# Kernel tuning notes

Hardware: AMD Instinct MI355X
Metric: run time of the kernel (lower is better)

## Reference

```python
import jax, jax.numpy as jnp
import numpy as np
from jax import lax

B, T, I, H = 64, 512, 256, 512


def _lstm_cell(inp, h, c, Wx, bx, Wh):
    # Wx: (4, in_dim, H), bx: (4, H), Wh: (4, H, H); gate order: i, f, o, g
    gates = jnp.einsum('bi,gio->bgo', inp, Wx) + jnp.einsum('bh,gho->bgo', h, Wh) + bx
    i_t = jax.nn.sigmoid(gates[:, 0])
    f_t = jax.nn.sigmoid(gates[:, 1])
    o_t = jax.nn.sigmoid(gates[:, 2])
    g_t = jnp.tanh(gates[:, 3])
    c_new = f_t * c + i_t * g_t
    h_new = o_t * jnp.tanh(c_new)
    return h_new, c_new


def setup_inputs() -> dict:
    key = jax.random.key(0)
    ks = jax.random.split(key, 9)
    s_i = 1.0 / np.sqrt(H)  # nn.Linear default init scale (uniform fan_in)
    s_x0 = 1.0 / np.sqrt(I)
    u = lambda k, shape, s: jax.random.uniform(k, shape, jnp.float32, -s, s)
    return {
        'x':   jax.random.normal(ks[0], (B, T, I), jnp.float32),
        'Wx0': u(ks[1], (4, I, H), s_x0),
        'bx0': u(ks[2], (4, H), s_x0),
        'Wh0': u(ks[3], (4, H, H), s_i),
        'Wx1': u(ks[4], (4, H, H), s_i),
        'bx1': u(ks[5], (4, H), s_i),
        'Wh1': u(ks[6], (4, H, H), s_i),
        'Wfc': u(ks[7], (H, 1), s_i),
        'bfc': u(ks[8], (1,), s_i),
    }


def reference(x, Wx0, bx0, Wh0, Wx1, bx1, Wh1, Wfc, bfc):
    b = x.shape[0]
    h = Wh0.shape[-1]
    zeros = jnp.zeros((b, h), x.dtype)
    carry0 = (zeros, zeros, zeros, zeros)  # h0, c0, h1, c1

    def step(carry, x_t):
        h0, c0, h1, c1 = carry
        h0, c0 = _lstm_cell(x_t, h0, c0, Wx0, bx0, Wh0)
        h1, c1 = _lstm_cell(h0, h1, c1, Wx1, bx1, Wh1)
        return (h0, c0, h1, c1), None

    x_t_major = jnp.swapaxes(x, 0, 1)  # (T, B, I)
    (h0, c0, h1, c1), _ = lax.scan(step, carry0, x_t_major)
    return h1 @ Wfc + bfc  # (B, 1)
```

## Files before the change

### kernel.cpp

```cpp
#include <hip/hip_runtime.h>
#include <stdint.h>

#define B_ 64
#define T_ 512
#define I_ 256
#define H_ 512
#define G0_ 128
#define G1_ 128
#define NTHR_ 512
#define D_ 8

typedef __attribute__((ext_vector_type(8))) short short8;
typedef __attribute__((ext_vector_type(4))) float float4v;
typedef __attribute__((ext_vector_type(4))) unsigned int uint4v;
typedef __attribute__((ext_vector_type(2))) unsigned int uint2v;

static_assert(sizeof(short8) == 16, "");

#define TILE_B 2048
#define SLOT_B ((size_t)4 * 16 * TILE_B)

__device__ __forceinline__ unsigned short f2bf(float x) {
  union { float f; uint32_t u; } v; v.f = x;
  uint32_t r = v.u + 0x7FFFu + ((v.u >> 16) & 1u);
  return (unsigned short)(r >> 16);
}
__device__ __forceinline__ float bf2f(unsigned short h) {
  union { uint32_t u; float f; } v; v.u = ((uint32_t)h) << 16; return v.f;
}
__device__ __forceinline__ void splitHL(float x, unsigned short& hi, unsigned short& lo) {
  hi = f2bf(x);
  lo = f2bf(x - bf2f(hi));
}

__device__ __forceinline__ size_t rbyte(int slot, int bg, int ht, int lane) {
  return ((size_t)slot * 64 + bg * 16 + ht) * TILE_B + (size_t)lane * 16;
}

__device__ __forceinline__ void wait_ge(const uint32_t* p, int tgt) {
  if (tgt <= 0) return;
  int it = 0;
  while ((int)__hip_atomic_load(p, __ATOMIC_RELAXED, __HIP_MEMORY_SCOPE_AGENT) < tgt) {
    __builtin_amdgcn_s_sleep(1);
    if (++it > 2000000) break;
  }
}

#define MFMA16(A, Bv, C) __builtin_amdgcn_mfma_f32_16x16x32_bf16(A, Bv, C, 0, 0, 0)

#define WAITV(n) do { \
    asm volatile("s_waitcnt vmcnt(" #n ")" ::: "memory"); \
    __builtin_amdgcn_sched_barrier(0); \
  } while (0)

template <int LAYER, bool FULL>
__device__ void run_layer(
    int a,
    const float* __restrict__ x,
    const float* __restrict__ Wxp, const float* __restrict__ bxp,
    const float* __restrict__ Whp,
    uint32_t* prog0, uint32_t* prog1,
    uint8_t* r0, uint8_t* r1,
    float* h1f,
    unsigned short* Wsh, float* red)
{
  constexpr int K1 = LAYER ? H_ : I_;
  constexpr int NT = (K1 + H_) / 32;
  constexpr int NTT = NT / 2;
  const int tid = threadIdx.x;
  const int lane = tid & 63;
  const int wid = tid >> 6;
  const int bg = wid & 3;
  const int kh = wid >> 2;
  const int qq = lane >> 4;
  const int cc = lane & 15;
  const int brow = bg * 16 + cc;

  short8 wlo[NTT];
  for (int pass = 0; pass < 2; ++pass) {
    for (int idx = tid; idx < NT * 512; idx += NTHR_) {
      int tile = idx >> 9, r = idx & 511, ln = r >> 3, j = r & 7;
      int k = tile * 32 + 4 * (ln >> 4) + (j & 3) + 16 * (j >> 2);
      int n = 4 * a + (ln & 3);
      int g = (ln & 15) >> 2;
      float wvv = (k < K1) ? Wxp[((size_t)g * K1 + k) * H_ + n]
                           : Whp[((size_t)g * H_ + (k - K1)) * H_ + n];
      unsigned short hi, lo; splitHL(wvv, hi, lo);
      Wsh[idx] = pass ? hi : lo;
    }
    __syncthreads();
    if (pass == 0) {
      #pragma unroll
      for (int tt = 0; tt < NTT; ++tt) {
        int tile = 2 * tt + kh;
        wlo[tt] = *(const short8*)(Wsh + tile * 512 + lane * 8);
      }
      __syncthreads();
    }
  }

  const float biasv = bxp[(size_t)(cc >> 2) * H_ + 4 * a + (cc & 3)];
  float cst[4] = {0.f, 0.f, 0.f, 0.f};

  uint32_t* myprog = LAYER ? prog1 : prog0;
  const bool ownw = FULL ? ((tid & 127) == a) : false;

  for (int t = 0; t < T_; ++t) {
    const int slotP = FULL ? t       : (t & (D_ - 1));
    const int slotC = FULL ? (t + 1) : ((t + 1) & (D_ - 1));
    float bv = (kh == 0) ? biasv : 0.f;
    float4v accA = {bv, bv, bv, bv};
    float4v accB = {0.f, 0.f, 0.f, 0.f};
    float4v accC = {0.f, 0.f, 0.f, 0.f};

    short8 hbuf[8], lbuf[8];
    uint4v xw0[4], xw1[4];

    auto issue_x = [&](int tt) {
      const int tile = 2 * tt + kh;
      const float* xp = x + ((size_t)brow * T_ + t) * I_ + tile * 32 + 4 * qq;
      asm volatile("global_load_dwordx4 %0, %2, off\n\t"
                   "global_load_dwordx4 %1, %2, off offset:64"
                   : "=&v"(xw0[tt]), "=&v"(xw1[tt]) : "v"(xp) : "memory");
    };
    auto proc_x = [&](int tt) {
      const int tile = 2 * tt + kh;
      short8 ahi, alo;
      #pragma unroll
      for (int j = 0; j < 4; ++j) {
        unsigned short hh, ll;
        splitHL(__uint_as_float(xw0[tt][j]), hh, ll); ahi[j] = (short)hh; alo[j] = (short)ll;
        splitHL(__uint_as_float(xw1[tt][j]), hh, ll); ahi[j + 4] = (short)hh; alo[j + 4] = (short)ll;
      }
      short8 bhi = *(const short8*)(Wsh + tile * 512 + lane * 8);
      accA = MFMA16(ahi, bhi, accA);
      accB = MFMA16(alo, bhi, accB);
      accC = MFMA16(ahi, wlo[tt], accC);
    };
    auto issue_ring = [&](int tt) {
      const int tile = 2 * tt + kh;
      const uint8_t* p;
      if (!LAYER)      p = r0 + rbyte(slotP, bg, tile - 8, lane);
      else if (tt < 8) p = r0 + rbyte(slotC, bg, tile, lane);
      else             p = r1 + rbyte(slotP, bg, tile - 16, lane);
      if constexpr (FULL) {
        asm volatile("global_load_dwordx4 %0, %2, off\n\t"
                     "global_load_dwordx4 %1, %2, off offset:1024"
                     : "=&v"(hbuf[tt & 7]), "=&v"(lbuf[tt & 7]) : "v"(p) : "memory");
      } else {
        asm volatile("global_load_dwordx4 %0, %2, off sc0 sc1\n\t"
                     "global_load_dwordx4 %1, %2, off offset:1024 sc0 sc1"
                     : "=&v"(hbuf[tt & 7]), "=&v"(lbuf[tt & 7]) : "v"(p) : "memory");
      }
    };
    auto proc_ring = [&](int tt) {
      const int tile = 2 * tt + kh;
      short8 bhi = *(const short8*)(Wsh + tile * 512 + lane * 8);
      accA = MFMA16(hbuf[tt & 7], bhi, accA);
      accB = MFMA16(lbuf[tt & 7], bhi, accB);
      accC = MFMA16(hbuf[tt & 7], wlo[tt], accC);
    };

    if constexpr (!LAYER) {
      issue_x(0); issue_x(1); issue_x(2); issue_x(3);
      WAITV(0);
      proc_x(0); proc_x(1); proc_x(2); proc_x(3);
      if constexpr (FULL) {
        if (!ownw) wait_ge(&prog0[tid], t);
      } else {
        if (tid < 128)      wait_ge(&prog0[tid], t);
        else if (tid < 256) wait_ge(&prog1[tid - 128], t - (D_ - 1));
      }
      __syncthreads();
      #pragma unroll
      for (int tt = 4; tt < 12; ++tt) issue_ring(tt);
      WAITV(8);
      proc_ring(4); proc_ring(5); proc_ring(6); proc_ring(7);
      WAITV(0);
      proc_ring(8); proc_ring(9); proc_ring(10); proc_ring(11);
    } else {
      if constexpr (FULL) {
        wait_ge(&prog0[tid], t + 1);
        if (!ownw) wait_ge(&prog1[tid], t);
      } else {
        if (tid < 128)      wait_ge(&prog0[tid], t + 1);
        else if (tid < 256) wait_ge(&prog1[tid - 128], t);
      }
      __syncthreads();
      #pragma unroll
      for (int tt = 0; tt < 8; ++tt) issue_ring(tt);
      WAITV(8);
      proc_ring(0); proc_ring(1); proc_ring(2); proc_ring(3);
      issue_ring(8); issue_ring(9); issue_ring(10); issue_ring(11);
      WAITV(8);
      proc_ring(4); proc_ring(5); proc_ring(6); proc_ring(7);
      issue_ring(12); issue_ring(13); issue_ring(14); issue_ring(15);
      WAITV(8);
      proc_ring(8); proc_ring(9); proc_ring(10); proc_ring(11);
      WAITV(0);
      proc_ring(12); proc_ring(13); proc_ring(14); proc_ring(15);
    }

    float4v acc = accA + accB + accC;

    if (kh == 1) *(float4v*)(red + ((bg << 6) + lane) * 4) = acc;
    __syncthreads();
    if (kh == 0) {
      acc += *(const float4v*)(red + ((bg << 6) + lane) * 4);

      const bool isg = cc >= 12;
      float av[4];
      #pragma unroll
      for (int i = 0; i < 4; ++i) {
        float xg = acc[i];
        float arg = isg ? xg + xg : xg;
        float e = __expf(-fabsf(arg));
        float s = (arg >= 0.f) ? 1.f / (1.f + e) : e / (1.f + e);
        av[i] = isg ? (s + s - 1.f) : s;
      }
      float hn[4];
      #pragma unroll
      for (int i = 0; i < 4; ++i) {
        float fv = __shfl_xor(av[i], 4);
        float ov = __shfl_xor(av[i], 8);
        float gv = __shfl_xor(av[i], 12);
        float cn = fv * cst[i] + av[i] * gv;
        cst[i] = cn;
        float e2 = __expf(-2.f * fabsf(cn));
        float th = (1.f - e2) / (1.f + e2);
        hn[i] = ov * ((cn >= 0.f) ? th : -th);
      }
      float v0[4], v1[4], v2[4], v3[4];
      #pragma unroll
      for (int d = 0; d < 4; ++d) {
        int src = (lane & 0x30) | d;
        v0[d] = __shfl(hn[0], src);
        v1[d] = __shfl(hn[1], src);
        v2[d] = __shfl(hn[2], src);
        v3[d] = __shfl(hn[3], src);
      }
      if (cc < 4) {
        unsigned short hh[4], ll[4]; float4v hf;
        #pragma unroll
        for (int d = 0; d < 4; ++d) {
          float hv = (cc == 0) ? v0[d] : (cc == 1) ? v1[d] : (cc == 2) ? v2[d] : v3[d];
          hf[d] = hv;
          splitHL(hv, hh[d], ll[d]);
        }
        uint2v hi2, lo2;
        hi2[0] = (uint32_t)hh[0] | ((uint32_t)hh[1] << 16);
        hi2[1] = (uint32_t)hh[2] | ((uint32_t)hh[3] << 16);
        lo2[0] = (uint32_t)ll[0] | ((uint32_t)ll[1] << 16);
        lo2[1] = (uint32_t)ll[2] | ((uint32_t)ll[3] << 16);
        uint8_t* dst = (LAYER ? r1 : r0)
                     + rbyte(slotC, bg, a >> 3, 16 * (a & 3) + 4 * qq + cc)
                     + 8 * ((a >> 2) & 1);
        asm volatile("global_store_dwordx2 %0, %1, off sc0 sc1\n\t"
                     "global_store_dwordx2 %0, %2, off offset:1024 sc0 sc1"
                     :: "v"(dst), "v"(hi2), "v"(lo2) : "memory");
        if (LAYER && t == T_ - 1) {
          float4v* hp = (float4v*)(h1f + (size_t)(bg * 16 + 4 * qq + cc) * H_ + 4 * a);
          asm volatile("global_store_dwordx4 %0, %1, off sc0 sc1"
                       :: "v"(hp), "v"(hf) : "memory");
        }
      }
    }
    if constexpr (FULL) {
      if (kh == 0) {
        asm volatile("s_waitcnt vmcnt(0)" ::: "memory");
        if (lane == 0)
          __hip_atomic_store(&myprog[bg * 128 + a], (uint32_t)(t + 1),
                             __ATOMIC_RELAXED, __HIP_MEMORY_SCOPE_AGENT);
      }
      __syncthreads();
    } else {
      asm volatile("s_waitcnt vmcnt(0)" ::: "memory");
      __syncthreads();
      if (tid == 0)
        __hip_atomic_store(&myprog[a], (uint32_t)(t + 1),
                           __ATOMIC_RELAXED, __HIP_MEMORY_SCOPE_AGENT);
    }
  }
}

template <bool FULL>
__global__ __launch_bounds__(NTHR_, 2) void lstm_persist(
    const float* __restrict__ x,
    const float* __restrict__ Wx0, const float* __restrict__ bx0, const float* __restrict__ Wh0,
    const float* __restrict__ Wx1, const float* __restrict__ bx1, const float* __restrict__ Wh1,
    uint32_t* prog0, uint32_t* prog1,
    uint8_t* ring0, uint8_t* ring1,
    float* h1f)
{
  __shared__ unsigned short Wsh[16384];
  __shared__ float red[1024];
  if (blockIdx.x < G0_)
    run_layer<0, FULL>(blockIdx.x, x, Wx0, bx0, Wh0, prog0, prog1, ring0, ring1, h1f, Wsh, red);
  else
    run_layer<1, FULL>(blockIdx.x - G0_, x, Wx1, bx1, Wh1, prog0, prog1, ring0, ring1, h1f, Wsh, red);
}

__global__ void fc_out(const float* __restrict__ h1f, const float* __restrict__ Wfc,
                       const float* __restrict__ bfc, float* __restrict__ out)
{
  int tid = threadIdx.x;
  int b = tid >> 3, p = tid & 7;
  const float* hp = h1f + (size_t)b * H_ + p * 64;
  const float* wp = Wfc + p * 64;
  float4v hv[16];
  #pragma unroll
  for (int q = 0; q < 16; ++q)
    asm volatile("global_load_dwordx4 %0, %1, off sc0 sc1"
                 : "=&v"(hv[q]) : "v"(hp + 4 * q) : "memory");
  asm volatile("s_waitcnt vmcnt(0)" ::: "memory");
  float s = 0.f;
  #pragma unroll
  for (int q = 0; q < 16; ++q) {
    float4v wv = *(const float4v*)(wp + 4 * q);
    s += hv[q][0] * wv[0] + hv[q][1] * wv[1] + hv[q][2] * wv[2] + hv[q][3] * wv[3];
  }
  s += __shfl_xor(s, 1);
  s += __shfl_xor(s, 2);
  s += __shfl_xor(s, 4);
  if (p == 0) out[b] = s + bfc[0];
}

extern "C" void kernel_launch(void* const* d_in, const int* in_sizes, int n_in,
                              void* d_out, int out_size, void* d_ws, size_t ws_size,
                              hipStream_t stream)
{
  const float* x   = (const float*)d_in[0];
  const float* Wx0 = (const float*)d_in[1];
  const float* bx0 = (const float*)d_in[2];
  const float* Wh0 = (const float*)d_in[3];
  const float* Wx1 = (const float*)d_in[4];
  const float* bx1 = (const float*)d_in[5];
  const float* Wh1 = (const float*)d_in[6];
  const float* Wfc = (const float*)d_in[7];
  const float* bfc = (const float*)d_in[8];

  uint8_t* ws = (uint8_t*)d_ws;
  const size_t RINGB_FULL = (size_t)(T_ + 1) * SLOT_B;
  const size_t RINGB_CYC  = (size_t)D_ * SLOT_B;
  const size_t NEED_FULL  = 4096 + 2 * RINGB_FULL + (size_t)B_ * H_ * 4;

  uint32_t* prog0 = (uint32_t*)ws;
  uint32_t* prog1 = (uint32_t*)(ws + 2048);

  if (ws_size >= NEED_FULL) {
    uint8_t* ring0 = ws + 4096;
    uint8_t* ring1 = ws + 4096 + RINGB_FULL;
    float* h1f = (float*)(ws + 4096 + 2 * RINGB_FULL);
    (void)hipMemsetAsync(ws, 0, 4096 + SLOT_B, stream);
    (void)hipMemsetAsync(ring1, 0, SLOT_B, stream);
    hipLaunchKernelGGL(lstm_persist<true>, dim3(G0_ + G1_), dim3(NTHR_), 0, stream,
                       x, Wx0, bx0, Wh0, Wx1, bx1, Wh1,
                       prog0, prog1, ring0, ring1, h1f);
    hipLaunchKernelGGL(fc_out, dim3(1), dim3(512), 0, stream,
                       h1f, Wfc, bfc, (float*)d_out);
  } else {
    uint8_t* ring0 = ws + 4096;
    uint8_t* ring1 = ws + 4096 + RINGB_CYC;
    float* h1f = (float*)(ws + 4096 + 2 * RINGB_CYC);
    (void)hipMemsetAsync(ws, 0, 4096 + 2 * RINGB_CYC, stream);
    hipLaunchKernelGGL(lstm_persist<false>, dim3(G0_ + G1_), dim3(NTHR_), 0, stream,
                       x, Wx0, bx0, Wh0, Wx1, bx1, Wh1,
                       prog0, prog1, ring0, ring1, h1f);
    hipLaunchKernelGGL(fc_out, dim3(1), dim3(512), 0, stream,
                       h1f, Wfc, bfc, (float*)d_out);
  }
}
```

Baseline: 3.005 ms.

## Drop K-split waves, sync per batch-group wave via vectorized flag polling

Each block now runs 4 waves of 256 threads instead of 8. Each wave owns one batch group and processes the full K range itself, so the LDS partial-sum reduction and all per-step __syncthreads are removed. Progress flags are tracked per (batch group, block), and a wave polls them with 64-bit loads plus __all, so waves synchronize only with the data they depend on. Hi and lo bf16 weight halves both move into LDS instead of keeping lo in registers. The trade-off is roughly twice the serial MFMA and load work per wave on the recurrent critical path, and fewer waves per CU to hide latency.

```diff
diff --git a/kernel.cpp b/kernel.cpp
--- a/kernel.cpp
+++ b/kernel.cpp
@@ -5,9 +5,7 @@
 #define T_ 512
 #define I_ 256
 #define H_ 512
-#define G0_ 128
-#define G1_ 128
-#define NTHR_ 512
+#define NTHR_ 256
 #define D_ 8
 
 typedef __attribute__((ext_vector_type(8))) short short8;
@@ -37,24 +35,16 @@
   return ((size_t)slot * 64 + bg * 16 + ht) * TILE_B + (size_t)lane * 16;
 }
 
-__device__ __forceinline__ void wait_ge(const uint32_t* p, int tgt) {
-  if (tgt <= 0) return;
-  int it = 0;
-  while ((int)__hip_atomic_load(p, __ATOMIC_RELAXED, __HIP_MEMORY_SCOPE_AGENT) < tgt) {
-    __builtin_amdgcn_s_sleep(1);
-    if (++it > 2000000) break;
-  }
-}
-
 #define MFMA16(A, Bv, C) __builtin_amdgcn_mfma_f32_16x16x32_bf16(A, Bv, C, 0, 0, 0)
 
 #define WAITV(n) do { \
     asm volatile("s_waitcnt vmcnt(" #n ")" ::: "memory"); \
     __builtin_amdgcn_sched_barrier(0); \
   } while (0)
+#define SB() __builtin_amdgcn_sched_barrier(0)
 
 template <int LAYER, bool FULL>
-__device__ void run_layer(
+__device__ void run_layer4(
     int a,
     const float* __restrict__ x,
     const float* __restrict__ Wxp, const float* __restrict__ bxp,
@@ -62,229 +52,213 @@
     uint32_t* prog0, uint32_t* prog1,
     uint8_t* r0, uint8_t* r1,
     float* h1f,
-    unsigned short* Wsh, float* red)
+    unsigned short* WshHi, unsigned short* WshLo)
 {
   constexpr int K1 = LAYER ? H_ : I_;
   constexpr int NT = (K1 + H_) / 32;
-  constexpr int NTT = NT / 2;
   const int tid = threadIdx.x;
   const int lane = tid & 63;
-  const int wid = tid >> 6;
-  const int bg = wid & 3;
-  const int kh = wid >> 2;
+  const int bg = tid >> 6;
   const int qq = lane >> 4;
   const int cc = lane & 15;
   const int brow = bg * 16 + cc;
 
-  short8 wlo[NTT];
-  for (int pass = 0; pass < 2; ++pass) {
-    for (int idx = tid; idx < NT * 512; idx += NTHR_) {
-      int tile = idx >> 9, r = idx & 511, ln = r >> 3, j = r & 7;
-      int k = tile * 32 + 4 * (ln >> 4) + (j & 3) + 16 * (j >> 2);
-      int n = 4 * a + (ln & 3);
-      int g = (ln & 15) >> 2;
-      float wvv = (k < K1) ? Wxp[((size_t)g * K1 + k) * H_ + n]
-                           : Whp[((size_t)g * H_ + (k - K1)) * H_ + n];
-      unsigned short hi, lo; splitHL(wvv, hi, lo);
-      Wsh[idx] = pass ? hi : lo;
-    }
-    __syncthreads();
-    if (pass == 0) {
-      #pragma unroll
-      for (int tt = 0; tt < NTT; ++tt) {
-        int tile = 2 * tt + kh;
-        wlo[tt] = *(const short8*)(Wsh + tile * 512 + lane * 8);
-      }
-      __syncthreads();
-    }
+  for (int idx = tid; idx < NT * 512; idx += NTHR_) {
+    int tile = idx >> 9, r = idx & 511, ln = r >> 3, j = r & 7;
+    int k = tile * 32 + 4 * (ln >> 4) + (j & 3) + 16 * (j >> 2);
+    int n = 4 * a + (ln & 3);
+    int g = (ln & 15) >> 2;
+    float wvv = (k < K1) ? Wxp[((size_t)g * K1 + k) * H_ + n]
+                         : Whp[((size_t)g * H_ + (k - K1)) * H_ + n];
+    unsigned short hi, lo; splitHL(wvv, hi, lo);
+    WshHi[idx] = hi; WshLo[idx] = lo;
   }
+  __syncthreads();
 
   const float biasv = bxp[(size_t)(cc >> 2) * H_ + 4 * a + (cc & 3)];
   float cst[4] = {0.f, 0.f, 0.f, 0.f};
 
-  uint32_t* myprog = LAYER ? prog1 : prog0;
-  const bool ownw = FULL ? ((tid & 127) == a) : false;
+  uint32_t* myflag = (LAYER ? prog1 : prog0) + bg * 128 + a;
+  const uint32_t* g0 = prog0 + bg * 128;
+  const uint32_t* g1 = prog1 + bg * 128;
+  const bool skip0 = (2 * lane == a), skip1 = (2 * lane + 1 == a);
+
+  auto poll = [&](const uint32_t* grp, int tgt, bool useSkip) {
+    if (tgt <= 0) return;
+    const unsigned long long* p = (const unsigned long long*)grp + lane;
+    int it = 0;
+    while (true) {
+      unsigned long long v = __hip_atomic_load(p, __ATOMIC_RELAXED,
+                                               __HIP_MEMORY_SCOPE_AGENT);
+      bool ok = ((useSkip && skip0) || (int)(uint32_t)v >= tgt) &&
+                ((useSkip && skip1) || (int)(uint32_t)(v >> 32) >= tgt);
+      if (__all((int)ok)) return;
+      __builtin_amdgcn_s_sleep(1);
+      if (++it > 2000000) return;
+    }
+  };
 
   for (int t = 0; t < T_; ++t) {
     const int slotP = FULL ? t       : (t & (D_ - 1));
     const int slotC = FULL ? (t + 1) : ((t + 1) & (D_ - 1));
-    float bv = (kh == 0) ? biasv : 0.f;
-    float4v accA = {bv, bv, bv, bv};
+    float4v accA = {biasv, biasv, biasv, biasv};
     float4v accB = {0.f, 0.f, 0.f, 0.f};
     float4v accC = {0.f, 0.f, 0.f, 0.f};
 
-    short8 hbuf[8], lbuf[8];
-    uint4v xw0[4], xw1[4];
-
-    auto issue_x = [&](int tt) {
-      const int tile = 2 * tt + kh;
-      const float* xp = x + ((size_t)brow * T_ + t) * I_ + tile * 32 + 4 * qq;
-      asm volatile("global_load_dwordx4 %0, %2, off\n\t"
-                   "global_load_dwordx4 %1, %2, off offset:64"
-                   : "=&v"(xw0[tt]), "=&v"(xw1[tt]) : "v"(xp) : "memory");
-    };
-    auto proc_x = [&](int tt) {
-      const int tile = 2 * tt + kh;
-      short8 ahi, alo;
-      #pragma unroll
-      for (int j = 0; j < 4; ++j) {
-        unsigned short hh, ll;
-        splitHL(__uint_as_float(xw0[tt][j]), hh, ll); ahi[j] = (short)hh; alo[j] = (short)ll;
-        splitHL(__uint_as_float(xw1[tt][j]), hh, ll); ahi[j + 4] = (short)hh; alo[j + 4] = (short)ll;
-      }
-      short8 bhi = *(const short8*)(Wsh + tile * 512 + lane * 8);
-      accA = MFMA16(ahi, bhi, accA);
-      accB = MFMA16(alo, bhi, accB);
-      accC = MFMA16(ahi, wlo[tt], accC);
-    };
-    auto issue_ring = [&](int tt) {
-      const int tile = 2 * tt + kh;
+    short8 hb[8], lb[8], hb2[8], lb2[8];
+
+    auto issue_tile = [&](short8* hd, short8* ld, int tile) {
       const uint8_t* p;
-      if (!LAYER)      p = r0 + rbyte(slotP, bg, tile - 8, lane);
-      else if (tt < 8) p = r0 + rbyte(slotC, bg, tile, lane);
-      else             p = r1 + rbyte(slotP, bg, tile - 16, lane);
+      if (!LAYER)        p = r0 + rbyte(slotP, bg, tile - 8, lane);
+      else if (tile < 16) p = r0 + rbyte(slotC, bg, tile, lane);
+      else                p = r1 + rbyte(slotP, bg, tile - 16, lane);
       if constexpr (FULL) {
         asm volatile("global_load_dwordx4 %0, %2, off\n\t"
                      "global_load_dwordx4 %1, %2, off offset:1024"
-                     : "=&v"(hbuf[tt & 7]), "=&v"(lbuf[tt & 7]) : "v"(p) : "memory");
+                     : "=&v"(*hd), "=&v"(*ld) : "v"(p) : "memory");
       } else {
         asm volatile("global_load_dwordx4 %0, %2, off sc0 sc1\n\t"
                      "global_load_dwordx4 %1, %2, off offset:1024 sc0 sc1"
-                     : "=&v"(hbuf[tt & 7]), "=&v"(lbuf[tt & 7]) : "v"(p) : "memory");
+                     : "=&v"(*hd), "=&v"(*ld) : "v"(p) : "memory");
       }
     };
-    auto proc_ring = [&](int tt) {
-      const int tile = 2 * tt + kh;
-      short8 bhi = *(const short8*)(Wsh + tile * 512 + lane * 8);
-      accA = MFMA16(hbuf[tt & 7], bhi, accA);
-      accB = MFMA16(lbuf[tt & 7], bhi, accB);
-      accC = MFMA16(hbuf[tt & 7], wlo[tt], accC);
+    auto proc_tile = [&](short8 h, short8 l, int tile) {
+      short8 bhi = *(const short8*)(WshHi + tile * 512 + lane * 8);
+      short8 blo = *(const short8*)(WshLo + tile * 512 + lane * 8);
+      accA = MFMA16(h, bhi, accA);
+      accB = MFMA16(l, bhi, accB);
+      accC = MFMA16(h, blo, accC);
     };
 
     if constexpr (!LAYER) {
-      issue_x(0); issue_x(1); issue_x(2); issue_x(3);
+      uint4v xw0[8], xw1[8];
+      #pragma unroll
+      for (int u = 0; u < 8; ++u) {
+        const float* xp = x + ((size_t)brow * T_ + t) * I_ + u * 32 + 4 * qq;
+        asm volatile("global_load_dwordx4 %0, %2, off\n\t"
+                     "global_load_dwordx4 %1, %2, off offset:64"
+                     : "=&v"(xw0[u]), "=&v"(xw1[u]) : "v"(xp) : "memory");
+      }
+      poll(g0, t, true);
+      if constexpr (!FULL) poll(g1, t - (D_ - 1), false);
       WAITV(0);
-      proc_x(0); proc_x(1); proc_x(2); proc_x(3);
-      if constexpr (FULL) {
-        if (!ownw) wait_ge(&prog0[tid], t);
-      } else {
-        if (tid < 128)      wait_ge(&prog0[tid], t);
-        else if (tid < 256) wait_ge(&prog1[tid - 128], t - (D_ - 1));
-      }
-      __syncthreads();
-      #pragma unroll
-      for (int tt = 4; tt < 12; ++tt) issue_ring(tt);
-      WAITV(8);
-      proc_ring(4); proc_ring(5); proc_ring(6); proc_ring(7);
+      #pragma unroll
+      for (int u = 0; u < 8; ++u) issue_tile(&hb[u],  &lb[u],  8 + u);
+      #pragma unroll
+      for (int u = 0; u < 8; ++u) issue_tile(&hb2[u], &lb2[u], 16 + u);
+      SB();
+      #pragma unroll
+      for (int u = 0; u < 8; ++u) {
+        short8 ahi, alo;
+        #pragma unroll
+        for (int j = 0; j < 4; ++j) {
+          unsigned short hh, ll;
+          splitHL(__uint_as_float(xw0[u][j]), hh, ll); ahi[j] = (short)hh; alo[j] = (short)ll;
+          splitHL(__uint_as_float(xw1[u][j]), hh, ll); ahi[j + 4] = (short)hh; alo[j + 4] = (short)ll;
+        }
+        proc_tile(ahi, alo, u);
+      }
+      WAITV(16);
+      #pragma unroll
+      for (int u = 0; u < 8; ++u) proc_tile(hb[u], lb[u], 8 + u);
       WAITV(0);
-      proc_ring(8); proc_ring(9); proc_ring(10); proc_ring(11);
+      #pragma unroll
+      for (int u = 0; u < 8; ++u) proc_tile(hb2[u], lb2[u], 16 + u);
     } else {
-      if constexpr (FULL) {
-        wait_ge(&prog0[tid], t + 1);
-        if (!ownw) wait_ge(&prog1[tid], t);
-      } else {
-        if (tid < 128)      wait_ge(&prog0[tid], t + 1);
-        else if (tid < 256) wait_ge(&prog1[tid - 128], t);
-      }
-      __syncthreads();
-      #pragma unroll
-      for (int tt = 0; tt < 8; ++tt) issue_ring(tt);
-      WAITV(8);
-      proc_ring(0); proc_ring(1); proc_ring(2); proc_ring(3);
-      issue_ring(8); issue_ring(9); issue_ring(10); issue_ring(11);
-      WAITV(8);
-      proc_ring(4); proc_ring(5); proc_ring(6); proc_ring(7);
-      issue_ring(12); issue_ring(13); issue_ring(14); issue_ring(15);
-      WAITV(8);
-      proc_ring(8); proc_ring(9); proc_ring(10); proc_ring(11);
+      short8 hb3[8], lb3[8], hb4[8], lb4[8];
+      poll(g0, t + 1, false);
+      SB();
+      #pragma unroll
+      for (int u = 0; u < 8; ++u) issue_tile(&hb[u],  &lb[u],  u);
+      #pragma unroll
+      for (int u = 0; u < 8; ++u) issue_tile(&hb2[u], &lb2[u], 8 + u);
+      poll(g1, t, true);
       WAITV(0);
-      proc_ring(12); proc_ring(13); proc_ring(14); proc_ring(15);
+      #pragma unroll
+      for (int u = 0; u < 8; ++u) issue_tile(&hb3[u], &lb3[u], 16 + u);
+      SB();
+      #pragma unroll
+      for (int u = 0; u < 8; ++u) proc_tile(hb[u], lb[u], u);
+      #pragma unroll
+      for (int u = 0; u < 8; ++u) issue_tile(&hb4[u], &lb4[u], 24 + u);
+      SB();
+      #pragma unroll
+      for (int u = 0; u < 8; ++u) proc_tile(hb2[u], lb2[u], 8 + u);
+      WAITV(16);
+      #pragma unroll
+      for (int u = 0; u < 8; ++u) proc_tile(hb3[u], lb3[u], 16 + u);
+      WAITV(0);
+      #pragma unroll
+      for (int u = 0; u < 8; ++u) proc_tile(hb4[u], lb4[u], 24 + u);
     }
 
     float4v acc = accA + accB + accC;
 
-    if (kh == 1) *(float4v*)(red + ((bg << 6) + lane) * 4) = acc;
-    __syncthreads();
-    if (kh == 0) {
-      acc += *(const float4v*)(red + ((bg << 6) + lane) * 4);
-
-      const bool isg = cc >= 12;
-      float av[4];
-      #pragma unroll
-      for (int i = 0; i < 4; ++i) {
-        float xg = acc[i];
-        float arg = isg ? xg + xg : xg;
-        float e = __expf(-fabsf(arg));
-        float s = (arg >= 0.f) ? 1.f / (1.f + e) : e / (1.f + e);
-        av[i] = isg ? (s + s - 1.f) : s;
-      }
-      float hn[4];
-      #pragma unroll
-      for (int i = 0; i < 4; ++i) {
-        float fv = __shfl_xor(av[i], 4);
-        float ov = __shfl_xor(av[i], 8);
-        float gv = __shfl_xor(av[i], 12);
-        float cn = fv * cst[i] + av[i] * gv;
-        cst[i] = cn;
-        float e2 = __expf(-2.f * fabsf(cn));
-        float th = (1.f - e2) / (1.f + e2);
-        hn[i] = ov * ((cn >= 0.f) ? th : -th);
-      }
-      float v0[4], v1[4], v2[4], v3[4];
+    const bool isg = cc >= 12;
+    float av[4];
+    #pragma unroll
+    for (int i = 0; i < 4; ++i) {
+      float xg = acc[i];
+      float arg = isg ? xg + xg : xg;
+      float e = __expf(-fabsf(arg));
+      float s = (arg >= 0.f) ? 1.f / (1.f + e) : e / (1.f + e);
+      av[i] = isg ? (s + s - 1.f) : s;
+    }
+    float hn[4];
+    #pragma unroll
+    for (int i = 0; i < 4; ++i) {
+      float fv = __shfl_xor(av[i], 4);
+      float ov = __shfl_xor(av[i], 8);
+      float gv = __shfl_xor(av[i], 12);
+      float cn = fv * cst[i] + av[i] * gv;
+      cst[i] = cn;
+      float e2 = __expf(-2.f * fabsf(cn));
+      float th = (1.f - e2) / (1.f + e2);
+      hn[i] = ov * ((cn >= 0.f) ? th : -th);
+    }
+    float v0[4], v1[4], v2[4], v3[4];
+    #pragma unroll
+    for (int d = 0; d < 4; ++d) {
+      int src = (lane & 0x30) | d;
+      v0[d] = __shfl(hn[0], src);
+      v1[d] = __shfl(hn[1], src);
+      v2[d] = __shfl(hn[2], src);
+      v3[d] = __shfl(hn[3], src);
+    }
+    if (cc < 4) {
+      unsigned short hh[4], ll[4]; float4v hf;
       #pragma unroll
       for (int d = 0; d < 4; ++d) {
-        int src = (lane & 0x30) | d;
-        v0[d] = __shfl(hn[0], src);
-        v1[d] = __shfl(hn[1], src);
-        v2[d] = __shfl(hn[2], src);
-        v3[d] = __shfl(hn[3], src);
-      }
-      if (cc < 4) {
-        unsigned short hh[4], ll[4]; float4v hf;
-        #pragma unroll
-        for (int d = 0; d < 4; ++d) {
-          float hv = (cc == 0) ? v0[d] : (cc == 1) ? v1[d] : (cc == 2) ? v2[d] : v3[d];
-          hf[d] = hv;
-          splitHL(hv, hh[d], ll[d]);
-        }
-        uint2v hi2, lo2;
-        hi2[0] = (uint32_t)hh[0] | ((uint32_t)hh[1] << 16);
-        hi2[1] = (uint32_t)hh[2] | ((uint32_t)hh[3] << 16);
-        lo2[0] = (uint32_t)ll[0] | ((uint32_t)ll[1] << 16);
-        lo2[1] = (uint32_t)ll[2] | ((uint32_t)ll[3] << 16);
-        uint8_t* dst = (LAYER ? r1 : r0)
-                     + rbyte(slotC, bg, a >> 3, 16 * (a & 3) + 4 * qq + cc)
-                     + 8 * ((a >> 2) & 1);
-        asm volatile("global_store_dwordx2 %0, %1, off sc0 sc1\n\t"
-                     "global_store_dwordx2 %0, %2, off offset:1024 sc0 sc1"
-                     :: "v"(dst), "v"(hi2), "v"(lo2) : "memory");
-        if (LAYER && t == T_ - 1) {
-          float4v* hp = (float4v*)(h1f + (size_t)(bg * 16 + 4 * qq + cc) * H_ + 4 * a);
-          asm volatile("global_store_dwordx4 %0, %1, off sc0 sc1"
-                       :: "v"(hp), "v"(hf) : "memory");
-        }
-      }
-    }
-    if constexpr (FULL) {
-      if (kh == 0) {
-        asm volatile("s_waitcnt vmcnt(0)" ::: "memory");
-        if (lane == 0)
-          __hip_atomic_store(&myprog[bg * 128 + a], (uint32_t)(t + 1),
-                             __ATOMIC_RELAXED, __HIP_MEMORY_SCOPE_AGENT);
-      }
-      __syncthreads();
-    } else {
-      asm volatile("s_waitcnt vmcnt(0)" ::: "memory");
-      __syncthreads();
-      if (tid == 0)
-        __hip_atomic_store(&myprog[a], (uint32_t)(t + 1),
-                           __ATOMIC_RELAXED, __HIP_MEMORY_SCOPE_AGENT);
-    }
+        float hv = (cc == 0) ? v0[d] : (cc == 1) ? v1[d] : (cc == 2) ? v2[d] : v3[d];
+        hf[d] = hv;
+        splitHL(hv, hh[d], ll[d]);
+      }
+      uint2v hi2, lo2;
+      hi2[0] = (uint32_t)hh[0] | ((uint32_t)hh[1] << 16);
+      hi2[1] = (uint32_t)hh[2] | ((uint32_t)hh[3] << 16);
+      lo2[0] = (uint32_t)ll[0] | ((uint32_t)ll[1] << 16);
+      lo2[1] = (uint32_t)ll[2] | ((uint32_t)ll[3] << 16);
+      uint8_t* dst = (LAYER ? r1 : r0)
+                   + rbyte(slotC, bg, a >> 3, 16 * (a & 3) + 4 * qq + cc)
+                   + 8 * ((a >> 2) & 1);
+      asm volatile("global_store_dwordx2 %0, %1, off sc0 sc1\n\t"
+                   "global_store_dwordx2 %0, %2, off offset:1024 sc0 sc1"
+                   :: "v"(dst), "v"(hi2), "v"(lo2) : "memory");
+      if (LAYER && t == T_ - 1) {
+        float4v* hp = (float4v*)(h1f + (size_t)(bg * 16 + 4 * qq + cc) * H_ + 4 * a);
+        asm volatile("global_store_dwordx4 %0, %1, off sc0 sc1"
+                     :: "v"(hp), "v"(hf) : "memory");
+      }
+    }
+    asm volatile("s_waitcnt vmcnt(0)" ::: "memory");
+    if (lane == 0)
+      __hip_atomic_store(myflag, (uint32_t)(t + 1),
+                         __ATOMIC_RELAXED, __HIP_MEMORY_SCOPE_AGENT);
   }
 }
 
 template <bool FULL>
-__global__ __launch_bounds__(NTHR_, 2) void lstm_persist(
+__global__ __launch_bounds__(NTHR_, 1) void lstm_persist4(
     const float* __restrict__ x,
     const float* __restrict__ Wx0, const float* __restrict__ bx0, const float* __restrict__ Wh0,
     const float* __restrict__ Wx1, const float* __restrict__ bx1, const float* __restrict__ Wh1,
@@ -292,12 +266,12 @@
     uint8_t* ring0, uint8_t* ring1,
     float* h1f)
 {
-  __shared__ unsigned short Wsh[16384];
-  __shared__ float red[1024];
-  if (blockIdx.x < G0_)
-    run_layer<0, FULL>(blockIdx.x, x, Wx0, bx0, Wh0, prog0, prog1, ring0, ring1, h1f, Wsh, red);
+  __shared__ unsigned short WshHi[16384];
+  __shared__ unsigned short WshLo[16384];
+  if (blockIdx.x < 128)
+    run_layer4<0, FULL>(blockIdx.x, x, Wx0, bx0, Wh0, prog0, prog1, ring0, ring1, h1f, WshHi, WshLo);
   else
-    run_layer<1, FULL>(blockIdx.x - G0_, x, Wx1, bx1, Wh1, prog0, prog1, ring0, ring1, h1f, Wsh, red);
+    run_layer4<1, FULL>(blockIdx.x - 128, x, Wx1, bx1, Wh1, prog0, prog1, ring0, ring1, h1f, WshHi, WshLo);
 }
 
 __global__ void fc_out(const float* __restrict__ h1f, const float* __restrict__ Wfc,
@@ -353,7 +327,7 @@
     float* h1f = (float*)(ws + 4096 + 2 * RINGB_FULL);
     (void)hipMemsetAsync(ws, 0, 4096 + SLOT_B, stream);
     (void)hipMemsetAsync(ring1, 0, SLOT_B, stream);
-    hipLaunchKernelGGL(lstm_persist<true>, dim3(G0_ + G1_), dim3(NTHR_), 0, stream,
+    hipLaunchKernelGGL(lstm_persist4<true>, dim3(256), dim3(NTHR_), 0, stream,
                        x, Wx0, bx0, Wh0, Wx1, bx1, Wh1,
                        prog0, prog1, ring0, ring1, h1f);
     hipLaunchKernelGGL(fc_out, dim3(1), dim3(512), 0, stream,
@@ -363,7 +337,7 @@
     uint8_t* ring1 = ws + 4096 + RINGB_CYC;
     float* h1f = (float*)(ws + 4096 + 2 * RINGB_CYC);
     (void)hipMemsetAsync(ws, 0, 4096 + 2 * RINGB_CYC, stream);
-    hipLaunchKernelGGL(lstm_persist<false>, dim3(G0_ + G1_), dim3(NTHR_), 0, stream,
+    hipLaunchKernelGGL(lstm_persist4<false>, dim3(256), dim3(NTHR_), 0, stream,
                        x, Wx0, bx0, Wh0, Wx1, bx1, Wh1,
                        prog0, prog1, ring0, ring1, h1f);
     hipLaunchKernelGGL(fc_out, dim3(1), dim3(512), 0, stream,
```

Result: slower. 4.568 ms (+52.0%).

## Overlap x loads with sync waits and split layer-1 waits per input half

Applied to the files above, without the earlier changes.

Layer 0 now issues its x loads before the progress wait and defers the bf16 split and MFMAs until after the ring loads are in flight, so global x latency overlaps the cross-block spin wait. In the FULL path, layer 1 first waits only on layer-0 progress, processes the h0 half of K, and only then waits on its own layer's previous-step progress before doing the recurrent half. This is meant to shorten the critical path of the inter-block dependency chain, at the cost of an extra __syncthreads per step and more live registers. The G0_/G1_ macros are also replaced with literal constants.

```diff
diff --git a/kernel.cpp b/kernel.cpp
--- a/kernel.cpp
+++ b/kernel.cpp
@@ -5,8 +5,6 @@
 #define T_ 512
 #define I_ 256
 #define H_ 512
-#define G0_ 128
-#define G1_ 128
 #define NTHR_ 512
 #define D_ 8
 
@@ -52,6 +50,7 @@
     asm volatile("s_waitcnt vmcnt(" #n ")" ::: "memory"); \
     __builtin_amdgcn_sched_barrier(0); \
   } while (0)
+#define SB() __builtin_amdgcn_sched_barrier(0)
 
 template <int LAYER, bool FULL>
 __device__ void run_layer(
@@ -108,41 +107,19 @@
   for (int t = 0; t < T_; ++t) {
     const int slotP = FULL ? t       : (t & (D_ - 1));
     const int slotC = FULL ? (t + 1) : ((t + 1) & (D_ - 1));
-    float bv = (kh == 0) ? biasv : 0.f;
+    const float bv = (kh == 0) ? biasv : 0.f;
     float4v accA = {bv, bv, bv, bv};
     float4v accB = {0.f, 0.f, 0.f, 0.f};
     float4v accC = {0.f, 0.f, 0.f, 0.f};
 
     short8 hbuf[8], lbuf[8];
-    uint4v xw0[4], xw1[4];
-
-    auto issue_x = [&](int tt) {
-      const int tile = 2 * tt + kh;
-      const float* xp = x + ((size_t)brow * T_ + t) * I_ + tile * 32 + 4 * qq;
-      asm volatile("global_load_dwordx4 %0, %2, off\n\t"
-                   "global_load_dwordx4 %1, %2, off offset:64"
-                   : "=&v"(xw0[tt]), "=&v"(xw1[tt]) : "v"(xp) : "memory");
-    };
-    auto proc_x = [&](int tt) {
-      const int tile = 2 * tt + kh;
-      short8 ahi, alo;
-      #pragma unroll
-      for (int j = 0; j < 4; ++j) {
-        unsigned short hh, ll;
-        splitHL(__uint_as_float(xw0[tt][j]), hh, ll); ahi[j] = (short)hh; alo[j] = (short)ll;
-        splitHL(__uint_as_float(xw1[tt][j]), hh, ll); ahi[j + 4] = (short)hh; alo[j + 4] = (short)ll;
-      }
-      short8 bhi = *(const short8*)(Wsh + tile * 512 + lane * 8);
-      accA = MFMA16(ahi, bhi, accA);
-      accB = MFMA16(alo, bhi, accB);
-      accC = MFMA16(ahi, wlo[tt], accC);
-    };
+
     auto issue_ring = [&](int tt) {
       const int tile = 2 * tt + kh;
       const uint8_t* p;
-      if (!LAYER)      p = r0 + rbyte(slotP, bg, tile - 8, lane);
-      else if (tt < 8) p = r0 + rbyte(slotC, bg, tile, lane);
-      else             p = r1 + rbyte(slotP, bg, tile - 16, lane);
+      if (!LAYER)         p = r0 + rbyte(slotP, bg, tile - 8, lane);
+      else if (tile < 16) p = r0 + rbyte(slotC, bg, tile, lane);
+      else                p = r1 + rbyte(slotP, bg, tile - 16, lane);
       if constexpr (FULL) {
         asm volatile("global_load_dwordx4 %0, %2, off\n\t"
                      "global_load_dwordx4 %1, %2, off offset:1024"
@@ -162,9 +139,14 @@
     };
 
     if constexpr (!LAYER) {
-      issue_x(0); issue_x(1); issue_x(2); issue_x(3);
-      WAITV(0);
-      proc_x(0); proc_x(1); proc_x(2); proc_x(3);
+      uint4v xw0[4], xw1[4];
+      #pragma unroll
+      for (int u = 0; u < 4; ++u) {
+        const float* xp = x + ((size_t)brow * T_ + t) * I_ + (2 * u + kh) * 32 + 4 * qq;
+        asm volatile("global_load_dwordx4 %0, %2, off\n\t"
+                     "global_load_dwordx4 %1, %2, off offset:64"
+                     : "=&v"(xw0[u]), "=&v"(xw1[u]) : "v"(xp) : "memory");
+      }
       if constexpr (FULL) {
         if (!ownw) wait_ge(&prog0[tid], t);
       } else {
@@ -174,6 +156,22 @@
       __syncthreads();
       #pragma unroll
       for (int tt = 4; tt < 12; ++tt) issue_ring(tt);
+      WAITV(16);
+      #pragma unroll
+      for (int u = 0; u < 4; ++u) {
+        short8 ahi, alo;
+        #pragma unroll
+        for (int j = 0; j < 4; ++j) {
+          unsigned short hh, ll;
+          splitHL(__uint_as_float(xw0[u][j]), hh, ll); ahi[j] = (short)hh; alo[j] = (short)ll;
+          splitHL(__uint_as_float(xw1[u][j]), hh, ll); ahi[j + 4] = (short)hh; alo[j + 4] = (short)ll;
+        }
+        const int tile = 2 * u + kh;
+        short8 bhi = *(const short8*)(Wsh + tile * 512 + lane * 8);
+        accA = MFMA16(ahi, bhi, accA);
+        accB = MFMA16(alo, bhi, accB);
+        accC = MFMA16(ahi, wlo[u], accC);
+      }
       WAITV(8);
       proc_ring(4); proc_ring(5); proc_ring(6); proc_ring(7);
       WAITV(0);
@@ -181,24 +179,38 @@
     } else {
       if constexpr (FULL) {
         wait_ge(&prog0[tid], t + 1);
+        __syncthreads();
+        #pragma unroll
+        for (int tt = 0; tt < 8; ++tt) issue_ring(tt);
+        WAITV(8);
+        proc_ring(0); proc_ring(1); proc_ring(2); proc_ring(3);
+        WAITV(0);
+        proc_ring(4); proc_ring(5); proc_ring(6); proc_ring(7);
         if (!ownw) wait_ge(&prog1[tid], t);
+        __syncthreads();
+        #pragma unroll
+        for (int tt = 8; tt < 16; ++tt) issue_ring(tt);
+        WAITV(8);
+        proc_ring(8); proc_ring(9); proc_ring(10); proc_ring(11);
+        WAITV(0);
+        proc_ring(12); proc_ring(13); proc_ring(14); proc_ring(15);
       } else {
         if (tid < 128)      wait_ge(&prog0[tid], t + 1);
         else if (tid < 256) wait_ge(&prog1[tid - 128], t);
-      }
-      __syncthreads();
-      #pragma unroll
-      for (int tt = 0; tt < 8; ++tt) issue_ring(tt);
-      WAITV(8);
-      proc_ring(0); proc_ring(1); proc_ring(2); proc_ring(3);
-      issue_ring(8); issue_ring(9); issue_ring(10); issue_ring(11);
-      WAITV(8);
-      proc_ring(4); proc_ring(5); proc_ring(6); proc_ring(7);
-      issue_ring(12); issue_ring(13); issue_ring(14); issue_ring(15);
-      WAITV(8);
-      proc_ring(8); proc_ring(9); proc_ring(10); proc_ring(11);
-      WAITV(0);
-      proc_ring(12); proc_ring(13); proc_ring(14); proc_ring(15);
+        __syncthreads();
+        #pragma unroll
+        for (int tt = 0; tt < 8; ++tt) issue_ring(tt);
+        WAITV(8);
+        proc_ring(0); proc_ring(1); proc_ring(2); proc_ring(3);
+        issue_ring(8); issue_ring(9); issue_ring(10); issue_ring(11);
+        WAITV(8);
+        proc_ring(4); proc_ring(5); proc_ring(6); proc_ring(7);
+        issue_ring(12); issue_ring(13); issue_ring(14); issue_ring(15);
+        WAITV(8);
+        proc_ring(8); proc_ring(9); proc_ring(10); proc_ring(11);
+        WAITV(0);
+        proc_ring(12); proc_ring(13); proc_ring(14); proc_ring(15);
+      }
     }
 
     float4v acc = accA + accB + accC;
@@ -294,10 +306,10 @@
 {
   __shared__ unsigned short Wsh[16384];
   __shared__ float red[1024];
-  if (blockIdx.x < G0_)
+  if (blockIdx.x < 128)
     run_layer<0, FULL>(blockIdx.x, x, Wx0, bx0, Wh0, prog0, prog1, ring0, ring1, h1f, Wsh, red);
   else
-    run_layer<1, FULL>(blockIdx.x - G0_, x, Wx1, bx1, Wh1, prog0, prog1, ring0, ring1, h1f, Wsh, red);
+    run_layer<1, FULL>(blockIdx.x - 128, x, Wx1, bx1, Wh1, prog0, prog1, ring0, ring1, h1f, Wsh, red);
 }
 
 __global__ void fc_out(const float* __restrict__ h1f, const float* __restrict__ Wfc,
@@ -353,7 +365,7 @@
     float* h1f = (float*)(ws + 4096 + 2 * RINGB_FULL);
     (void)hipMemsetAsync(ws, 0, 4096 + SLOT_B, stream);
     (void)hipMemsetAsync(ring1, 0, SLOT_B, stream);
-    hipLaunchKernelGGL(lstm_persist<true>, dim3(G0_ + G1_), dim3(NTHR_), 0, stream,
+    hipLaunchKernelGGL(lstm_persist<true>, dim3(256), dim3(NTHR_), 0, stream,
                        x, Wx0, bx0, Wh0, Wx1, bx1, Wh1,
                        prog0, prog1, ring0, ring1, h1f);
     hipLaunchKernelGGL(fc_out, dim3(1), dim3(512), 0, stream,
@@ -363,7 +375,7 @@
     uint8_t* ring1 = ws + 4096 + RINGB_CYC;
     float* h1f = (float*)(ws + 4096 + 2 * RINGB_CYC);
     (void)hipMemsetAsync(ws, 0, 4096 + 2 * RINGB_CYC, stream);
-    hipLaunchKernelGGL(lstm_persist<false>, dim3(G0_ + G1_), dim3(NTHR_), 0, stream,
+    hipLaunchKernelGGL(lstm_persist<false>, dim3(256), dim3(NTHR_), 0, stream,
                        x, Wx0, bx0, Wh0, Wx1, bx1, Wh1,
                        prog0, prog1, ring0, ring1, h1f);
     hipLaunchKernelGGL(fc_out, dim3(1), dim3(512), 0, stream,
```

Measured after the change: 3.126 ms. 4.0% more time.
